# Kernel optimization log

Measured on AMD Instinct MI355X. Metric: run time of the kernel, lower is better.

Reference implementation:

```python
import jax, jax.numpy as jnp
import numpy as np

B, S, D, H = 8, 1024, 256, 8
HD = D // H
EPS = 1e-5
NEG = -1000000000.0


def setup_inputs() -> dict:
    key = jax.random.key(0)
    ks = jax.random.split(key, 12)
    s = 1.0 / np.sqrt(D)
    inp = {
        "q": jax.random.normal(ks[0], (B, S, D), jnp.float32),
        "kv_mask": jax.random.randint(ks[1], (B, S), 0, 2) > 0,
        "attn_bias": jax.random.normal(ks[2], (B, S, S, H), jnp.float32),
        "Wq": jax.random.normal(ks[3], (D, D), jnp.float32) * s,
        "bq": jax.random.normal(ks[4], (D,), jnp.float32) * s,
        "Wk": jax.random.normal(ks[5], (D, D), jnp.float32) * s,
        "bk": jax.random.normal(ks[6], (D,), jnp.float32) * s,
        "Wv": jax.random.normal(ks[7], (D, D), jnp.float32) * s,
        "bv": jax.random.normal(ks[8], (D,), jnp.float32) * s,
        "gamma": jnp.ones((D,), jnp.float32),
        "beta": jnp.zeros((D,), jnp.float32),
        "Wo": jax.random.normal(ks[9], (D, D), jnp.float32) * s,
        "bo": jax.random.normal(ks[10], (D,), jnp.float32) * s,
    }
    return inp


def reference(q, kv_mask, attn_bias, Wq, bq, Wk, bk, Wv, bv, gamma, beta, Wo, bo):
    b, s, d = q.shape
    # merge_masks: q_mask all True -> merged = kv_mask broadcast over query dim
    merged = jnp.broadcast_to(kv_mask[:, None, None, :], (b, 1, s, s))  # [b,1,s,s]
    # additive float mask: (~mask)*-1e9 + bias permuted to [b,h,q,k]
    add_mask = (~merged).astype(q.dtype) * NEG + jnp.transpose(attn_bias, (0, 3, 1, 2))
    # projections (torch Linear: x @ W.T + b)
    qh = (q @ Wq.T + bq).reshape(b, s, H, HD).transpose(0, 2, 1, 3)  # [b,h,s,hd]
    kh = (q @ Wk.T + bk).reshape(b, s, H, HD).transpose(0, 2, 1, 3)
    vh = (q @ Wv.T + bv).reshape(b, s, H, HD).transpose(0, 2, 1, 3)
    scores = jnp.einsum("bhqd,bhkd->bhqk", qh, kh) / np.sqrt(HD) + add_mask
    attn = jax.nn.softmax(scores, axis=-1)
    a = jnp.einsum("bhqk,bhkd->bhqd", attn, vh)  # [b,h,s,hd]
    a = a.transpose(0, 2, 1, 3).reshape(b, s, d)
    # LayerNorm (eps=1e-5)
    mu = a.mean(-1, keepdims=True)
    var = ((a - mu) ** 2).mean(-1, keepdims=True)
    a = (a - mu) / jnp.sqrt(var + EPS) * gamma + beta
    return a @ Wo.T + bo
```

## Files before the change

### kernel.cpp

```cpp
#include <hip/hip_runtime.h>
#include <hip/hip_bf16.h>


static constexpr int SEQ = 1024;
static constexpr float SCL  = 0.17677669529663687f;
static constexpr float NEGV = -1000000000.0f;

typedef __attribute__((ext_vector_type(8))) __bf16 bf8v;
typedef __attribute__((ext_vector_type(4))) float  f4v;

__device__ __forceinline__ f4v mfma16(bf8v a, bf8v b, f4v c) {
  return __builtin_amdgcn_mfma_f32_16x16x32_bf16(a, b, c, 0, 0, 0);
}
__device__ __forceinline__ unsigned short bfbits(float f) {
  __hip_bfloat16 hbf = __float2bfloat16(f);
  unsigned short u; __builtin_memcpy(&u, &hbf, 2); return u;
}
__device__ __forceinline__ float bf2f(unsigned short u) {
  unsigned x = ((unsigned)u) << 16; float f; __builtin_memcpy(&f, &x, 4); return f;
}
__device__ __forceinline__ void lds_barrier() {
  __builtin_amdgcn_sched_barrier(0);
  asm volatile("s_waitcnt lgkmcnt(0)" ::: "memory");
  __builtin_amdgcn_s_barrier();
  __builtin_amdgcn_sched_barrier(0);
}

__global__ __launch_bounds__(256) void prep_kernel(
    const float* __restrict__ q, const float* __restrict__ Wq,
    const float* __restrict__ Wk, const float* __restrict__ Wv,
    const float* __restrict__ Wo, const int* __restrict__ km,
    __hip_bfloat16* __restrict__ q_bf, __hip_bfloat16* __restrict__ w_bf,
    float* __restrict__ mskf)
{
  const int NQ4 = (8192 * 256) / 4;
  const int NW4 = 65536 / 4;
  int t = threadIdx.x;

  if (blockIdx.x == 2304) {
    __shared__ int isbool;
    if (t == 0) isbool = 0;
    __syncthreads();
    const unsigned* u = (const unsigned*)km;
    int any = 0;
    for (int i = t; i < 2048; i += 256)
      if (u[i] & ~1u) any = 1;
    if (any) isbool = 1;
    __syncthreads();
    const unsigned char* b8 = (const unsigned char*)km;
    for (int i = t; i < 8192; i += 256) {
      int mv = isbool ? (int)b8[i] : km[i];
      mskf[i] = mv ? 0.f : NEGV;
    }
    return;
  }

  int i = blockIdx.x * 256 + t;
  const float4* src; __hip_bfloat16* dst;
  if (i < NQ4) {
    src = (const float4*)q + i;
    dst = q_bf + (long)i * 4;
  } else {
    int j = i - NQ4; int w = j >> 14; int o4 = j & (NW4 - 1);
    const float* sp = (w == 0) ? Wq : (w == 1) ? Wk : (w == 2) ? Wv : Wo;
    src = (const float4*)sp + o4;
    dst = w_bf + w * 65536 + o4 * 4;
  }
  float4 v = *src;
  ushort4 pk;
  pk.x = bfbits(v.x); pk.y = bfbits(v.y); pk.z = bfbits(v.z); pk.w = bfbits(v.w);
  *reinterpret_cast<ushort4*>(dst) = pk;
}

__global__ __launch_bounds__(256) void qkv_gemm(
    const __hip_bfloat16* __restrict__ q_bf, const __hip_bfloat16* __restrict__ w_bf,
    const float* __restrict__ bq, const float* __restrict__ bk,
    const float* __restrict__ bv,
    __hip_bfloat16* __restrict__ qh, __hip_bfloat16* __restrict__ kh,
    __hip_bfloat16* __restrict__ vt)
{
  int z = blockIdx.z;
  int w = threadIdx.x >> 6;
  int l = threadIdx.x & 63, lr = l & 15, lg = l >> 4;

  const __hip_bfloat16 *A, *Bm; const float* bias; __hip_bfloat16* out;
  long ldOut; int m0, n0;
  if (z < 2) {
    A = q_bf; Bm = w_bf + z * 65536; bias = z ? bk : bq; out = z ? kh : qh;
    ldOut = 256;
    m0 = blockIdx.x * 64; n0 = blockIdx.y * 128 + w * 32;
  } else {
    A = w_bf + 2 * 65536; Bm = q_bf; bias = bv; out = vt; ldOut = 8192;
    int bid = blockIdx.y * 128 + blockIdx.x;
    m0 = (bid >> 6) * 64; n0 = (bid & 63) * 128 + w * 32;
  }

  f4v acc[4][2];
#pragma unroll
  for (int mt = 0; mt < 4; ++mt)
#pragma unroll
    for (int nt = 0; nt < 2; ++nt) acc[mt][nt] = f4v{0.f, 0.f, 0.f, 0.f};

  const __hip_bfloat16* Ab = A  + (long)(m0 + lr) * 256 + lg * 8;
  const __hip_bfloat16* Bb = Bm + (long)(n0 + lr) * 256 + lg * 8;
#pragma unroll
  for (int k0 = 0; k0 < 256; k0 += 32) {
    bf8v af[4], bfr[2];
#pragma unroll
    for (int mt = 0; mt < 4; ++mt)
      af[mt] = *reinterpret_cast<const bf8v*>(Ab + (long)mt * 16 * 256 + k0);
#pragma unroll
    for (int nt = 0; nt < 2; ++nt)
      bfr[nt] = *reinterpret_cast<const bf8v*>(Bb + (long)nt * 16 * 256 + k0);
#pragma unroll
    for (int mt = 0; mt < 4; ++mt)
#pragma unroll
      for (int nt = 0; nt < 2; ++nt)
        acc[mt][nt] = mfma16(af[mt], bfr[nt], acc[mt][nt]);
  }

#pragma unroll
  for (int mt = 0; mt < 4; ++mt) {
    int mrow = m0 + mt * 16 + lg * 4;
#pragma unroll
    for (int nt = 0; nt < 2; ++nt) {
      int ncol = n0 + nt * 16 + lr;
#pragma unroll
      for (int r = 0; r < 4; ++r) {
        float v = acc[mt][nt][r] + ((z == 2) ? bias[mrow + r] : bias[ncol]);
        if (z == 0) v *= SCL;
        out[(long)(mrow + r) * ldOut + ncol] = __float2bfloat16(v);
      }
    }
  }
}

__global__ __launch_bounds__(512, 2) void attn_kernel(
    const __hip_bfloat16* __restrict__ qh, const __hip_bfloat16* __restrict__ kh,
    const __hip_bfloat16* __restrict__ vt, const float* __restrict__ bias,
    const float* __restrict__ mskf, const __hip_bfloat16* __restrict__ wob,
    const float* __restrict__ gamma, const float* __restrict__ beta,
    const float* __restrict__ bo, float* __restrict__ outp)
{
  __shared__ __align__(16) char smem[51712];
  __hip_bfloat16* bsm = (__hip_bfloat16*)smem;
  __hip_bfloat16* psm = (__hip_bfloat16*)(smem + 37376);
  float* msk = (float*)(smem + 47616);
  float* osm = (float*)smem;
  __hip_bfloat16* ansm = (__hip_bfloat16*)(smem + 33792);

  int bb = blockIdx.x & 7;
  int qt = blockIdx.x >> 3;
  int h  = threadIdx.x >> 6;
  int l  = threadIdx.x & 63, lr = l & 15, lg = l >> 4;
  int q0 = qt * 32;
  long bS = (long)bb * SEQ;
  int t = threadIdx.x;
  int sq = t >> 4, kp = (t >> 1) & 7, hh = t & 1;

  for (int i = t; i < 1024; i += 512) msk[i] = mskf[bS + i];

  bf8v qf[2];
#pragma unroll
  for (int qs = 0; qs < 2; ++qs)
    qf[qs] = *reinterpret_cast<const bf8v*>(
        qh + (bS + q0 + qs * 16 + lr) * 256 + h * 32 + lg * 8);

  f4v o[2][2];
  float lsum[2] = {0.f, 0.f};
#pragma unroll
  for (int qs = 0; qs < 2; ++qs)
#pragma unroll
    for (int nt = 0; nt < 2; ++nt) o[qs][nt] = f4v{0.f, 0.f, 0.f, 0.f};

  const float* bgb = bias + (bS + q0 + sq) * 8192L + 4 * hh;

  auto loadBias = [&](int tile, float4 (&br)[4]) {
    int kb = tile * 32;
#pragma unroll
    for (int kk = 0; kk < 4; ++kk)
      br[kk] = *reinterpret_cast<const float4*>(bgb + (long)(kb + 4 * kp + kk) * 8);
  };
  auto cvtWrite = [&](int buf, const float4 (&br)[4], int tile) {
    int kb = tile * 32;
    float mk[4];
#pragma unroll
    for (int kk = 0; kk < 4; ++kk) mk[kk] = msk[kb + 4 * kp + kk];
    __hip_bfloat16* bp = bsm + buf * 9344 + sq * 292 + 4 * kp;
    float w_[4][4] = {{br[0].x, br[0].y, br[0].z, br[0].w},
                      {br[1].x, br[1].y, br[1].z, br[1].w},
                      {br[2].x, br[2].y, br[2].z, br[2].w},
                      {br[3].x, br[3].y, br[3].z, br[3].w}};
#pragma unroll
    for (int i = 0; i < 4; ++i) {
      ushort4 hb;
      hb.x = bfbits(w_[0][i] + mk[0]); hb.y = bfbits(w_[1][i] + mk[1]);
      hb.z = bfbits(w_[2][i] + mk[2]); hb.w = bfbits(w_[3][i] + mk[3]);
      *reinterpret_cast<ushort4*>(bp + (4 * hh + i) * 36) = hb;
    }
  };
  auto loadKV = [&](int tile, bf8v (&kf)[2], bf8v (&vf)[2]) {
    int kbase = tile * 32;
#pragma unroll
    for (int nt = 0; nt < 2; ++nt)
      kf[nt] = *reinterpret_cast<const bf8v*>(
          kh + (bS + kbase + nt * 16 + lr) * 256 + h * 32 + lg * 8);
#pragma unroll
    for (int n2 = 0; n2 < 2; ++n2)
      vf[n2] = *reinterpret_cast<const bf8v*>(
          vt + (long)(h * 32 + n2 * 16 + lr) * 8192 + bS + kbase + lg * 8);
  };

  auto compute = [&](int kt, const bf8v (&kf)[2], const bf8v (&vf)[2]) {
    const __hip_bfloat16* bbp = bsm + (kt & 1) * 9344;
#pragma unroll
    for (int qs = 0; qs < 2; ++qs) {
      f4v z4 = f4v{0.f, 0.f, 0.f, 0.f};
      f4v s0 = mfma16(kf[0], qf[qs], z4);
      f4v s1 = mfma16(kf[1], qf[qs], z4);

      const __hip_bfloat16* bp = bbp + (qs * 16 + lr) * 292 + h * 36;
      ushort4 b0 = *reinterpret_cast<const ushort4*>(bp + lg * 4);
      ushort4 b1 = *reinterpret_cast<const ushort4*>(bp + 16 + lg * 4);

      float p[8];
      p[0] = __expf(s0[0] + bf2f(b0.x)); p[1] = __expf(s0[1] + bf2f(b0.y));
      p[2] = __expf(s0[2] + bf2f(b0.z)); p[3] = __expf(s0[3] + bf2f(b0.w));
      p[4] = __expf(s1[0] + bf2f(b1.x)); p[5] = __expf(s1[1] + bf2f(b1.y));
      p[6] = __expf(s1[2] + bf2f(b1.z)); p[7] = __expf(s1[3] + bf2f(b1.w));
      lsum[qs] += ((p[0] + p[1]) + (p[2] + p[3])) + ((p[4] + p[5]) + (p[6] + p[7]));

      __hip_bfloat16* pw = psm + h * 640 + lr * 40;
      ushort4 pk0, pk1;
      pk0.x = bfbits(p[0]); pk0.y = bfbits(p[1]); pk0.z = bfbits(p[2]); pk0.w = bfbits(p[3]);
      pk1.x = bfbits(p[4]); pk1.y = bfbits(p[5]); pk1.z = bfbits(p[6]); pk1.w = bfbits(p[7]);
      *reinterpret_cast<ushort4*>(pw + 4 * lg)      = pk0;
      *reinterpret_cast<ushort4*>(pw + 16 + 4 * lg) = pk1;

      bf8v pa = *reinterpret_cast<const bf8v*>(psm + h * 640 + lr * 40 + lg * 8);
      o[qs][0] = mfma16(pa, vf[0], o[qs][0]);
      o[qs][1] = mfma16(pa, vf[1], o[qs][1]);
    }
  };

  float4 brA[4], brB[4];
  bf8v kfA[2], vfA[2], kfB[2], vfB[2];

  loadBias(0, brA);
  loadBias(1, brB);
  loadKV(0, kfA, vfA);
  lds_barrier();
  cvtWrite(0, brA, 0);
  lds_barrier();

  for (int m = 0; m < 16; ++m) {
    { int kt = 2 * m;
      if (kt + 2 < 32) loadBias(kt + 2, brA);
      loadKV(kt + 1, kfB, vfB);
      compute(kt, kfA, vfA);
      cvtWrite(1, brB, kt + 1);
      lds_barrier(); }
    { int kt = 2 * m + 1;
      if (kt + 2 < 32) { loadBias(kt + 2, brB); loadKV(kt + 1, kfA, vfA); }
      compute(kt, kfB, vfB);
      if (kt + 1 < 32) cvtWrite(0, brA, kt + 1);
      lds_barrier(); }
  }

  float rinv[2];
#pragma unroll
  for (int qs = 0; qs < 2; ++qs) {
    float s = lsum[qs];
    s += __shfl_xor(s, 16);
    s += __shfl_xor(s, 32);
    rinv[qs] = 1.f / s;
  }

  __syncthreads();
#pragma unroll
  for (int qs = 0; qs < 2; ++qs)
#pragma unroll
    for (int r = 0; r < 4; ++r) {
      float invr = __shfl(rinv[qs], lg * 4 + r);
      int row = qs * 16 + lg * 4 + r;
      osm[row * 264 + h * 32 + lr]      = o[qs][0][r] * invr;
      osm[row * 264 + h * 32 + 16 + lr] = o[qs][1][r] * invr;
    }
  __syncthreads();

  {
    int row = t >> 4;
    int c16 = (t & 15) * 16;
    float vv[16]; float sm = 0.f, sq2 = 0.f;
#pragma unroll
    for (int j4 = 0; j4 < 4; ++j4) {
      float4 v4 = *reinterpret_cast<const float4*>(osm + row * 264 + c16 + j4 * 4);
      vv[j4 * 4 + 0] = v4.x; vv[j4 * 4 + 1] = v4.y;
      vv[j4 * 4 + 2] = v4.z; vv[j4 * 4 + 3] = v4.w;
      sm += v4.x + v4.y + v4.z + v4.w;
      sq2 += v4.x * v4.x + v4.y * v4.y + v4.z * v4.z + v4.w * v4.w;
    }
#pragma unroll
    for (int mm = 1; mm < 16; mm <<= 1) { sm += __shfl_xor(sm, mm); sq2 += __shfl_xor(sq2, mm); }
    float mean = sm * (1.f / 256.f);
    float var  = sq2 * (1.f / 256.f) - mean * mean;
    float rstd = rsqrtf(var + 1e-5f);
#pragma unroll
    for (int j4 = 0; j4 < 4; ++j4) {
      float4 g = *reinterpret_cast<const float4*>(gamma + c16 + j4 * 4);
      float4 b = *reinterpret_cast<const float4*>(beta + c16 + j4 * 4);
      ushort4 pk;
      pk.x = bfbits((vv[j4 * 4 + 0] - mean) * rstd * g.x + b.x);
      pk.y = bfbits((vv[j4 * 4 + 1] - mean) * rstd * g.y + b.y);
      pk.z = bfbits((vv[j4 * 4 + 2] - mean) * rstd * g.z + b.z);
      pk.w = bfbits((vv[j4 * 4 + 3] - mean) * rstd * g.w + b.w);
      *reinterpret_cast<ushort4*>(&ansm[row * 264 + c16 + j4 * 4]) = pk;
    }
  }
  __syncthreads();

#pragma unroll
  for (int qs = 0; qs < 2; ++qs) {
    f4v acc2[2];
    acc2[0] = f4v{0.f, 0.f, 0.f, 0.f}; acc2[1] = f4v{0.f, 0.f, 0.f, 0.f};
#pragma unroll
    for (int k0 = 0; k0 < 256; k0 += 32) {
      bf8v afr = *reinterpret_cast<const bf8v*>(&ansm[(qs * 16 + lr) * 264 + lg * 8 + k0]);
#pragma unroll
      for (int nt = 0; nt < 2; ++nt) {
        bf8v bfrg = *reinterpret_cast<const bf8v*>(
            wob + (long)(h * 32 + nt * 16 + lr) * 256 + lg * 8 + k0);
        acc2[nt] = mfma16(afr, bfrg, acc2[nt]);
      }
    }
#pragma unroll
    for (int nt = 0; nt < 2; ++nt) {
      int ocol = h * 32 + nt * 16 + lr;
      float bov = bo[ocol];
#pragma unroll
      for (int r = 0; r < 4; ++r) {
        int orow = q0 + qs * 16 + lg * 4 + r;
        outp[(bS + orow) * 256 + ocol] = acc2[nt][r] + bov;
      }
    }
  }
}

extern "C" void kernel_launch(void* const* d_in, const int* in_sizes, int n_in,
                              void* d_out, int out_size, void* d_ws, size_t ws_size,
                              hipStream_t stream) {
  const float* q   = (const float*)d_in[0];
  const int*   km  = (const int*)d_in[1];
  const float* bias = (const float*)d_in[2];
  const float* Wq = (const float*)d_in[3];
  const float* bq = (const float*)d_in[4];
  const float* Wk = (const float*)d_in[5];
  const float* bk = (const float*)d_in[6];
  const float* Wv = (const float*)d_in[7];
  const float* bv = (const float*)d_in[8];
  const float* gamma = (const float*)d_in[9];
  const float* beta  = (const float*)d_in[10];
  const float* Wo = (const float*)d_in[11];
  const float* bo = (const float*)d_in[12];

  char* wsb = (char*)d_ws;
  __hip_bfloat16* q_bf = (__hip_bfloat16*)(wsb + 0);
  __hip_bfloat16* qh   = (__hip_bfloat16*)(wsb + (4  << 20));
  __hip_bfloat16* kh   = (__hip_bfloat16*)(wsb + (8  << 20));
  __hip_bfloat16* vt   = (__hip_bfloat16*)(wsb + (12 << 20));
  __hip_bfloat16* wbf  = (__hip_bfloat16*)(wsb + (16 << 20));
  float*          mskf = (float*)         (wsb + (17 << 20));
  __hip_bfloat16* wob  = wbf + 196608;

  prep_kernel<<<2305, 256, 0, stream>>>(q, Wq, Wk, Wv, Wo, km, q_bf, wbf, mskf);
  qkv_gemm<<<dim3(128, 2, 3), 256, 0, stream>>>(q_bf, wbf, bq, bk, bv, qh, kh, vt);
  attn_kernel<<<256, 512, 0, stream>>>(qh, kh, vt, bias, mskf, wob,
                                       gamma, beta, bo, (float*)d_out);
}
```

Baseline: 114.5 us.

## Double key tile per phase to 64 and drop K/V register prefetch

The attention main loop now processes 64 keys per phase instead of 32. The bias staging buffers, probability LDS tile and register bias prefetch grow to match, and shared memory nearly doubles to about 92 KB. This halves the number of barriers and loop iterations and gives more MFMA work per sync. K/V fragments are now loaded just before use instead of being software-prefetched one tile ahead, which may expose global load latency. The larger LDS footprint likely drops occupancy from two 512-thread blocks per CU.

```diff
diff --git a/kernel.cpp b/kernel.cpp
--- a/kernel.cpp
+++ b/kernel.cpp
@@ -142,10 +142,10 @@
     const float* __restrict__ gamma, const float* __restrict__ beta,
     const float* __restrict__ bo, float* __restrict__ outp)
 {
-  __shared__ __align__(16) char smem[51712];
+  __shared__ __align__(16) char smem[92672];
   __hip_bfloat16* bsm = (__hip_bfloat16*)smem;
-  __hip_bfloat16* psm = (__hip_bfloat16*)(smem + 37376);
-  float* msk = (float*)(smem + 47616);
+  __hip_bfloat16* psm = (__hip_bfloat16*)(smem + 70144);
+  float* msk = (float*)(smem + 88576);
   float* osm = (float*)smem;
   __hip_bfloat16* ansm = (__hip_bfloat16*)(smem + 33792);
 
@@ -175,95 +175,108 @@
 
   const float* bgb = bias + (bS + q0 + sq) * 8192L + 4 * hh;
 
-  auto loadBias = [&](int tile, float4 (&br)[4]) {
-    int kb = tile * 32;
-#pragma unroll
-    for (int kk = 0; kk < 4; ++kk)
-      br[kk] = *reinterpret_cast<const float4*>(bgb + (long)(kb + 4 * kp + kk) * 8);
+  auto loadBias = [&](int phase, float4 (&br)[8]) {
+    int kb = phase * 64;
+#pragma unroll
+    for (int kk = 0; kk < 8; ++kk)
+      br[kk] = *reinterpret_cast<const float4*>(bgb + (long)(kb + 8 * kp + kk) * 8);
   };
-  auto cvtWrite = [&](int buf, const float4 (&br)[4], int tile) {
-    int kb = tile * 32;
-    float mk[4];
-#pragma unroll
-    for (int kk = 0; kk < 4; ++kk) mk[kk] = msk[kb + 4 * kp + kk];
-    __hip_bfloat16* bp = bsm + buf * 9344 + sq * 292 + 4 * kp;
-    float w_[4][4] = {{br[0].x, br[0].y, br[0].z, br[0].w},
-                      {br[1].x, br[1].y, br[1].z, br[1].w},
-                      {br[2].x, br[2].y, br[2].z, br[2].w},
-                      {br[3].x, br[3].y, br[3].z, br[3].w}};
+  auto cvtWrite = [&](int buf, const float4 (&br)[8], int phase) {
+    int kb = phase * 64;
+    float mk[8];
+#pragma unroll
+    for (int kk = 0; kk < 8; ++kk) mk[kk] = msk[kb + 8 * kp + kk];
+    __hip_bfloat16* bp = bsm + buf * 17536 + sq * 548 + 8 * kp;
 #pragma unroll
     for (int i = 0; i < 4; ++i) {
-      ushort4 hb;
-      hb.x = bfbits(w_[0][i] + mk[0]); hb.y = bfbits(w_[1][i] + mk[1]);
-      hb.z = bfbits(w_[2][i] + mk[2]); hb.w = bfbits(w_[3][i] + mk[3]);
-      *reinterpret_cast<ushort4*>(bp + (4 * hh + i) * 36) = hb;
+      unsigned short w8[8];
+#pragma unroll
+      for (int kk = 0; kk < 8; ++kk) {
+        float vv = (i == 0) ? br[kk].x : (i == 1) ? br[kk].y
+                 : (i == 2) ? br[kk].z : br[kk].w;
+        w8[kk] = bfbits(vv + mk[kk]);
+      }
+      __builtin_memcpy(bp + (4 * hh + i) * 68, w8, 16);
     }
   };
-  auto loadKV = [&](int tile, bf8v (&kf)[2], bf8v (&vf)[2]) {
-    int kbase = tile * 32;
-#pragma unroll
-    for (int nt = 0; nt < 2; ++nt)
-      kf[nt] = *reinterpret_cast<const bf8v*>(
-          kh + (bS + kbase + nt * 16 + lr) * 256 + h * 32 + lg * 8);
+  auto loadKV = [&](int phase, bf8v (&kf)[4], bf8v (&vf)[2][2]) {
+    int kbase = phase * 64;
+#pragma unroll
+    for (int u = 0; u < 4; ++u)
+      kf[u] = *reinterpret_cast<const bf8v*>(
+          kh + (bS + kbase + u * 16 + lr) * 256 + h * 32 + lg * 8);
 #pragma unroll
     for (int n2 = 0; n2 < 2; ++n2)
-      vf[n2] = *reinterpret_cast<const bf8v*>(
-          vt + (long)(h * 32 + n2 * 16 + lr) * 8192 + bS + kbase + lg * 8);
+#pragma unroll
+      for (int s2 = 0; s2 < 2; ++s2)
+        vf[n2][s2] = *reinterpret_cast<const bf8v*>(
+            vt + (long)(h * 32 + n2 * 16 + lr) * 8192 + bS + kbase + s2 * 32 + lg * 8);
   };
 
-  auto compute = [&](int kt, const bf8v (&kf)[2], const bf8v (&vf)[2]) {
-    const __hip_bfloat16* bbp = bsm + (kt & 1) * 9344;
+  auto compute = [&](int phase, const bf8v (&kf)[4], const bf8v (&vf)[2][2]) {
+    const __hip_bfloat16* bbp = bsm + (phase & 1) * 17536;
 #pragma unroll
     for (int qs = 0; qs < 2; ++qs) {
       f4v z4 = f4v{0.f, 0.f, 0.f, 0.f};
-      f4v s0 = mfma16(kf[0], qf[qs], z4);
-      f4v s1 = mfma16(kf[1], qf[qs], z4);
-
-      const __hip_bfloat16* bp = bbp + (qs * 16 + lr) * 292 + h * 36;
-      ushort4 b0 = *reinterpret_cast<const ushort4*>(bp + lg * 4);
-      ushort4 b1 = *reinterpret_cast<const ushort4*>(bp + 16 + lg * 4);
-
-      float p[8];
-      p[0] = __expf(s0[0] + bf2f(b0.x)); p[1] = __expf(s0[1] + bf2f(b0.y));
-      p[2] = __expf(s0[2] + bf2f(b0.z)); p[3] = __expf(s0[3] + bf2f(b0.w));
-      p[4] = __expf(s1[0] + bf2f(b1.x)); p[5] = __expf(s1[1] + bf2f(b1.y));
-      p[6] = __expf(s1[2] + bf2f(b1.z)); p[7] = __expf(s1[3] + bf2f(b1.w));
-      lsum[qs] += ((p[0] + p[1]) + (p[2] + p[3])) + ((p[4] + p[5]) + (p[6] + p[7]));
-
-      __hip_bfloat16* pw = psm + h * 640 + lr * 40;
-      ushort4 pk0, pk1;
-      pk0.x = bfbits(p[0]); pk0.y = bfbits(p[1]); pk0.z = bfbits(p[2]); pk0.w = bfbits(p[3]);
-      pk1.x = bfbits(p[4]); pk1.y = bfbits(p[5]); pk1.z = bfbits(p[6]); pk1.w = bfbits(p[7]);
-      *reinterpret_cast<ushort4*>(pw + 4 * lg)      = pk0;
-      *reinterpret_cast<ushort4*>(pw + 16 + 4 * lg) = pk1;
-
-      bf8v pa = *reinterpret_cast<const bf8v*>(psm + h * 640 + lr * 40 + lg * 8);
-      o[qs][0] = mfma16(pa, vf[0], o[qs][0]);
-      o[qs][1] = mfma16(pa, vf[1], o[qs][1]);
+      f4v s[4];
+#pragma unroll
+      for (int u = 0; u < 4; ++u) s[u] = mfma16(kf[u], qf[qs], z4);
+
+      const __hip_bfloat16* bp = bbp + (qs * 16 + lr) * 548 + h * 68;
+      float v[16];
+#pragma unroll
+      for (int u = 0; u < 4; ++u) {
+        ushort4 b4 = *reinterpret_cast<const ushort4*>(bp + u * 16 + lg * 4);
+        v[u * 4 + 0] = s[u][0] + bf2f(b4.x);
+        v[u * 4 + 1] = s[u][1] + bf2f(b4.y);
+        v[u * 4 + 2] = s[u][2] + bf2f(b4.z);
+        v[u * 4 + 3] = s[u][3] + bf2f(b4.w);
+      }
+
+      float p[16]; float ts = 0.f;
+#pragma unroll
+      for (int i = 0; i < 16; ++i) { p[i] = __expf(v[i]); ts += p[i]; }
+      lsum[qs] += ts;
+
+      __hip_bfloat16* pw = psm + h * 1152 + lr * 72;
+#pragma unroll
+      for (int u = 0; u < 4; ++u) {
+        ushort4 pk;
+        pk.x = bfbits(p[u * 4 + 0]); pk.y = bfbits(p[u * 4 + 1]);
+        pk.z = bfbits(p[u * 4 + 2]); pk.w = bfbits(p[u * 4 + 3]);
+        *reinterpret_cast<ushort4*>(pw + u * 16 + lg * 4) = pk;
+      }
+
+#pragma unroll
+      for (int s2 = 0; s2 < 2; ++s2) {
+        bf8v pa = *reinterpret_cast<const bf8v*>(psm + h * 1152 + lr * 72 + s2 * 32 + lg * 8);
+        o[qs][0] = mfma16(pa, vf[0][s2], o[qs][0]);
+        o[qs][1] = mfma16(pa, vf[1][s2], o[qs][1]);
+      }
     }
   };
 
-  float4 brA[4], brB[4];
-  bf8v kfA[2], vfA[2], kfB[2], vfB[2];
+  float4 brA[8], brB[8];
+  bf8v kf[4], vf[2][2];
 
   loadBias(0, brA);
   loadBias(1, brB);
-  loadKV(0, kfA, vfA);
   lds_barrier();
   cvtWrite(0, brA, 0);
   lds_barrier();
 
-  for (int m = 0; m < 16; ++m) {
-    { int kt = 2 * m;
-      if (kt + 2 < 32) loadBias(kt + 2, brA);
-      loadKV(kt + 1, kfB, vfB);
-      compute(kt, kfA, vfA);
-      cvtWrite(1, brB, kt + 1);
+  for (int m = 0; m < 8; ++m) {
+    { int p = 2 * m;
+      if (p + 2 < 16) loadBias(p + 2, brA);
+      loadKV(p, kf, vf);
+      compute(p, kf, vf);
+      cvtWrite(1, brB, p + 1);
       lds_barrier(); }
-    { int kt = 2 * m + 1;
-      if (kt + 2 < 32) { loadBias(kt + 2, brB); loadKV(kt + 1, kfA, vfA); }
-      compute(kt, kfB, vfB);
-      if (kt + 1 < 32) cvtWrite(0, brA, kt + 1);
+    { int p = 2 * m + 1;
+      if (p + 2 < 16) loadBias(p + 2, brB);
+      loadKV(p, kf, vf);
+      compute(p, kf, vf);
+      if (p + 1 < 16) cvtWrite(0, brA, p + 1);
       lds_barrier(); }
   }
 
```

Measured after the change: 126.4 us. 1.1x slower.
